# Optimization experiments

Measured on AMD Instinct MI355X. Metric: run time of the kernel, lower is better.

The kernel has to match this reference:

```python
import jax, jax.numpy as jnp
import numpy as np


def setup_inputs() -> dict:
    key = jax.random.key(0)
    k1, k2, k3, k4 = jax.random.split(key, 4)
    B, T, C, H = 4, 2048, 1024, 64
    x = jax.random.normal(k1, (B, T, C), dtype=jnp.float32)
    # Linear(embed_dim, head_size, bias=False) weights, stored as [C, H] for x @ W
    s = 1.0 / np.sqrt(C)
    Wq = jax.random.normal(k2, (C, H), dtype=jnp.float32) * s
    Wk = jax.random.normal(k3, (C, H), dtype=jnp.float32) * s
    Wv = jax.random.normal(k4, (C, H), dtype=jnp.float32) * s
    return {"x": x, "Wq": Wq, "Wk": Wk, "Wv": Wv}


def reference(x, Wq, Wk, Wv):
    B, T, C = x.shape
    q = x @ Wq  # [B, T, H]
    k = x @ Wk
    v = x @ Wv
    # NOTE: original scales by embed_dim**-0.5 (C), not head_size**-0.5
    scale = C ** (-0.5)
    wei = jnp.einsum("bqh,bkh->bqk", q, k) * scale  # [B, T, T]
    causal = jnp.tril(jnp.ones((T, T), dtype=bool))
    wei = jnp.where(causal, wei, -jnp.inf)
    wei = jax.nn.softmax(wei, axis=-1)
    # dropout_rate = 0 -> identity
    out = jnp.einsum("bqk,bkh->bqh", wei, v)  # [B, T, H]
    return out
```

## Files before the change

### kernel.cpp

```cpp
#include <hip/hip_runtime.h>
#include <cmath>

#define B_ 4
#define T_ 2048
#define C_ 1024
#define H_ 64
#define SCALE_ 0.03125f
#define NEG_ -3.0e38f

typedef __attribute__((ext_vector_type(4))) float f32x4;
typedef __attribute__((ext_vector_type(8))) short s16x8;
typedef __attribute__((ext_vector_type(4))) unsigned short u16x4;

__device__ inline unsigned short f2bf(float f) {
    union { float f; unsigned u; } v; v.f = f;
    unsigned r = v.u + 0x7FFFu + ((v.u >> 16) & 1u);
    return (unsigned short)(r >> 16);
}

#define LDK 72

__global__ __launch_bounds__(256) void proj_mfma(
    const float* __restrict__ x, const float* __restrict__ Wq,
    const float* __restrict__ Wk, const float* __restrict__ Wv,
    unsigned short* __restrict__ qb, unsigned short* __restrict__ kb,
    unsigned short* __restrict__ vt)
{
    __shared__ unsigned short As[64 * LDK];
    __shared__ unsigned short Bs[64 * LDK];

    const int t = threadIdx.x;
    const int lane = t & 63;
    const int w = t >> 6;
    const int blk = blockIdx.x;
    const int mat = blk % 3;
    const int row0 = (blk / 3) * 64;

    const float* W = (mat == 0) ? Wq : (mat == 1) ? Wk : Wv;

    const int wr = (w >> 1) * 32;
    const int wc = (w & 1) * 32;
    const int fr = lane & 15;
    const int ko = (lane >> 4) * 8;

    f32x4 acc[2][2];
    #pragma unroll
    for (int mi = 0; mi < 2; ++mi)
        #pragma unroll
        for (int ni = 0; ni < 2; ++ni)
            acc[mi][ni] = (f32x4){0.f, 0.f, 0.f, 0.f};

    const int bcol = t & 63;
    const int bkg  = (t >> 6) * 4;

    for (int kt = 0; kt < C_; kt += 64) {
        __syncthreads();
        #pragma unroll
        for (int i = 0; i < 4; ++i) {
            int idx = t + i * 256;
            int r = idx >> 4, kc = (idx & 15) * 4;
            f32x4 xv = *(const f32x4*)(x + (size_t)(row0 + r) * C_ + kt + kc);
            u16x4 bv;
            bv.x = f2bf(xv.x); bv.y = f2bf(xv.y); bv.z = f2bf(xv.z); bv.w = f2bf(xv.w);
            *(u16x4*)&As[r * LDK + kc] = bv;
        }
        #pragma unroll
        for (int i = 0; i < 4; ++i) {
            int kk0 = bkg + i * 16;
            u16x4 bv;
            bv.x = f2bf(W[(size_t)(kt + kk0 + 0) * H_ + bcol]);
            bv.y = f2bf(W[(size_t)(kt + kk0 + 1) * H_ + bcol]);
            bv.z = f2bf(W[(size_t)(kt + kk0 + 2) * H_ + bcol]);
            bv.w = f2bf(W[(size_t)(kt + kk0 + 3) * H_ + bcol]);
            *(u16x4*)&Bs[bcol * LDK + kk0] = bv;
        }
        __syncthreads();
        #pragma unroll
        for (int ks = 0; ks < 2; ++ks) {
            s16x8 a0 = *(const s16x8*)&As[(wr + fr) * LDK + ks * 32 + ko];
            s16x8 a1 = *(const s16x8*)&As[(wr + 16 + fr) * LDK + ks * 32 + ko];
            s16x8 b0 = *(const s16x8*)&Bs[(wc + fr) * LDK + ks * 32 + ko];
            s16x8 b1 = *(const s16x8*)&Bs[(wc + 16 + fr) * LDK + ks * 32 + ko];
            acc[0][0] = __builtin_amdgcn_mfma_f32_16x16x32_bf16(a0, b0, acc[0][0], 0, 0, 0);
            acc[0][1] = __builtin_amdgcn_mfma_f32_16x16x32_bf16(a0, b1, acc[0][1], 0, 0, 0);
            acc[1][0] = __builtin_amdgcn_mfma_f32_16x16x32_bf16(a1, b0, acc[1][0], 0, 0, 0);
            acc[1][1] = __builtin_amdgcn_mfma_f32_16x16x32_bf16(a1, b1, acc[1][1], 0, 0, 0);
        }
    }

    if (mat < 2) {
        unsigned short* outb = (mat == 0) ? qb : kb;
        #pragma unroll
        for (int mi = 0; mi < 2; ++mi)
            #pragma unroll
            for (int ni = 0; ni < 2; ++ni)
                #pragma unroll
                for (int j = 0; j < 4; ++j) {
                    int row = row0 + wr + mi * 16 + (lane >> 4) * 4 + j;
                    int col = wc + ni * 16 + fr;
                    outb[(size_t)row * H_ + col] = f2bf(acc[mi][ni][j]);
                }
    } else {
        __syncthreads();
        #pragma unroll
        for (int mi = 0; mi < 2; ++mi)
            #pragma unroll
            for (int ni = 0; ni < 2; ++ni)
                #pragma unroll
                for (int j = 0; j < 4; ++j) {
                    int r = wr + mi * 16 + (lane >> 4) * 4 + j;
                    int cc = wc + ni * 16 + fr;
                    As[cc * LDK + r] = f2bf(acc[mi][ni][j]);
                }
        __syncthreads();
        int h = t >> 2, c0 = (t & 3) * 16;
        int bb = row0 >> 11, trow = row0 & 2047;
        s16x8 v0 = *(const s16x8*)&As[h * LDK + c0];
        s16x8 v1 = *(const s16x8*)&As[h * LDK + c0 + 8];
        size_t dst = (size_t)bb * H_ * T_ + (size_t)h * T_ + trow + c0;
        *(s16x8*)&vt[dst] = v0;
        *(s16x8*)&vt[dst + 8] = v1;
    }
}

__global__ __launch_bounds__(512, 4) void attn_mfma(
    const unsigned short* __restrict__ qb, const unsigned short* __restrict__ kb,
    const unsigned short* __restrict__ vt, float* __restrict__ out)
{
    __shared__ alignas(16) unsigned short Ps[8][1024];
    __shared__ float Os[8][16][68];
    __shared__ float Mm[8][16];
    __shared__ float Ll[8][16];

    const int t = threadIdx.x, lane = t & 63, w = t >> 6;
    const int fr = lane & 15, hi4 = lane >> 4;
    const int blk = blockIdx.x;
    const int b = blk & 3;
    const int qt = 127 - (blk >> 2);
    const int qbase = qt * 16;

    const unsigned short* qp = qb + ((size_t)b * T_ + qbase) * H_;
    const unsigned short* kp = kb + (size_t)b * T_ * H_;
    const unsigned short* vp = vt + (size_t)b * H_ * T_;

    s16x8 qf0 = *(const s16x8*)&qp[fr * H_ + hi4 * 8];
    s16x8 qf1 = *(const s16x8*)&qp[fr * H_ + 32 + hi4 * 8];

    const int nt = (qbase + 79) >> 6;
    const int per = (nt + 7) >> 3;
    const int tb = w * per;
    int te = tb + per; if (te > nt) te = nt;

    float m = NEG_, l = 0.f;
    f32x4 o[4];
    #pragma unroll
    for (int hf = 0; hf < 4; ++hf) o[hf] = (f32x4){0.f, 0.f, 0.f, 0.f};

    unsigned short* P = &Ps[w][0];
    const int swz = (fr & 3) << 4;
    const int qrow = qbase + fr;

    for (int kt = tb; kt < te; ++kt) {
        const int kt0 = kt << 6;

        f32x4 s[4];
        #pragma unroll
        for (int n = 0; n < 4; ++n) {
            const unsigned short* kr = &kp[(size_t)(kt0 + n * 16 + fr) * H_ + hi4 * 8];
            s16x8 kf0 = *(const s16x8*)kr;
            s16x8 kf1 = *(const s16x8*)(kr + 32);
            f32x4 a = (f32x4){0.f, 0.f, 0.f, 0.f};
            a = __builtin_amdgcn_mfma_f32_16x16x32_bf16(kf0, qf0, a, 0, 0, 0);
            a = __builtin_amdgcn_mfma_f32_16x16x32_bf16(kf1, qf1, a, 0, 0, 0);
            s[n] = a;
        }

        if (kt0 + 63 > qbase) {
            #pragma unroll
            for (int n = 0; n < 4; ++n)
                #pragma unroll
                for (int j = 0; j < 4; ++j) {
                    int key = kt0 + n * 16 + hi4 * 4 + j;
                    float sv = s[n][j] * SCALE_;
                    s[n][j] = (key > qrow) ? NEG_ : sv;
                }
        } else {
            #pragma unroll
            for (int n = 0; n < 4; ++n)
                #pragma unroll
                for (int j = 0; j < 4; ++j) s[n][j] *= SCALE_;
        }

        float mx01 = fmaxf(fmaxf(s[0][0], s[0][1]), fmaxf(s[0][2], s[0][3]));
        float mx23 = fmaxf(fmaxf(s[1][0], s[1][1]), fmaxf(s[1][2], s[1][3]));
        float mx45 = fmaxf(fmaxf(s[2][0], s[2][1]), fmaxf(s[2][2], s[2][3]));
        float mx67 = fmaxf(fmaxf(s[3][0], s[3][1]), fmaxf(s[3][2], s[3][3]));
        float mx = fmaxf(fmaxf(mx01, mx23), fmaxf(mx45, mx67));
        mx = fmaxf(mx, __shfl_xor(mx, 16));
        mx = fmaxf(mx, __shfl_xor(mx, 32));

        float mn = fmaxf(m, mx);
        float corr = __expf(m - mn);
        m = mn;
        float sum = 0.f;
        #pragma unroll
        for (int n = 0; n < 4; ++n)
            #pragma unroll
            for (int j = 0; j < 4; ++j) {
                float p = __expf(s[n][j] - mn);
                s[n][j] = p; sum += p;
            }
        sum += __shfl_xor(sum, 16);
        sum += __shfl_xor(sum, 32);
        l = l * corr + sum;

        #pragma unroll
        for (int j = 0; j < 4; ++j) {
            float cj = __shfl(corr, (lane & 48) + hi4 * 4 + j);
            o[0][j] *= cj; o[1][j] *= cj; o[2][j] *= cj; o[3][j] *= cj;
        }

        #pragma unroll
        for (int n = 0; n < 4; ++n) {
            u16x4 pk;
            pk.x = f2bf(s[n][0]); pk.y = f2bf(s[n][1]);
            pk.z = f2bf(s[n][2]); pk.w = f2bf(s[n][3]);
            *(u16x4*)&P[fr * 64 + ((n * 16 + hi4 * 4) ^ swz)] = pk;
        }
        s16x8 pa0 = *(const s16x8*)&P[fr * 64 + ((hi4 * 8) ^ swz)];
        s16x8 pa1 = *(const s16x8*)&P[fr * 64 + ((32 + hi4 * 8) ^ swz)];

        #pragma unroll
        for (int hf = 0; hf < 4; ++hf) {
            const unsigned short* vr = &vp[(size_t)(hf * 16 + fr) * T_ + kt0 + hi4 * 8];
            s16x8 vf0 = *(const s16x8*)vr;
            s16x8 vf1 = *(const s16x8*)(vr + 32);
            o[hf] = __builtin_amdgcn_mfma_f32_16x16x32_bf16(pa0, vf0, o[hf], 0, 0, 0);
            o[hf] = __builtin_amdgcn_mfma_f32_16x16x32_bf16(pa1, vf1, o[hf], 0, 0, 0);
        }
    }

    if (hi4 == 0) { Mm[w][fr] = m; Ll[w][fr] = l; }
    #pragma unroll
    for (int hf = 0; hf < 4; ++hf)
        #pragma unroll
        for (int j = 0; j < 4; ++j)
            Os[w][hi4 * 4 + j][hf * 16 + fr] = o[hf][j];
    __syncthreads();

    if (t < 256) {
        int qq = t >> 4, h0 = (t & 15) * 4;
        float M = NEG_;
        #pragma unroll
        for (int s8 = 0; s8 < 8; ++s8) M = fmaxf(M, Mm[s8][qq]);
        float L = 0.f;
        f32x4 r = (f32x4){0.f, 0.f, 0.f, 0.f};
        #pragma unroll
        for (int s8 = 0; s8 < 8; ++s8) {
            float e = __expf(Mm[s8][qq] - M);
            L += Ll[s8][qq] * e;
            f32x4 osv = *(const f32x4*)&Os[s8][qq][h0];
            r.x = fmaf(osv.x, e, r.x);
            r.y = fmaf(osv.y, e, r.y);
            r.z = fmaf(osv.z, e, r.z);
            r.w = fmaf(osv.w, e, r.w);
        }
        float il = 1.0f / L;
        r.x *= il; r.y *= il; r.z *= il; r.w *= il;
        *(f32x4*)&out[((size_t)b * T_ + qbase + qq) * H_ + h0] = r;
    }
}

extern "C" void kernel_launch(void* const* d_in, const int* in_sizes, int n_in,
                              void* d_out, int out_size, void* d_ws, size_t ws_size,
                              hipStream_t stream) {
    const float* x  = (const float*)d_in[0];
    const float* Wq = (const float*)d_in[1];
    const float* Wk = (const float*)d_in[2];
    const float* Wv = (const float*)d_in[3];
    float* outp = (float*)d_out;

    unsigned short* base = (unsigned short*)d_ws;
    unsigned short* qbw = base;
    unsigned short* kbw = base + 524288;
    unsigned short* vtw = base + 1048576;

    proj_mfma<<<(B_ * T_ / 64) * 3, 256, 0, stream>>>(x, Wq, Wk, Wv, qbw, kbw, vtw);
    attn_mfma<<<B_ * (T_ / 16), 512, 0, stream>>>(qbw, kbw, vtw, outp);
}
```

Baseline: 49.57 us.

## Fold softmax scale into exp2, skip rescale under threshold, prefetch V fragments

The softmax scale and log2(e) are folded into one constant, so the kernel uses exp2f with an FMA and no longer scales the raw scores. The running max is updated and O/l rescaled only when some lane's new max exceeds the stored max by more than a threshold (lazy rescaling, FA4-style). V fragments are loaded before the softmax so their latency overlaps with the exp work, and bf16 conversion now uses the library intrinsic. The lazy rescale lets unnormalized values grow up to roughly 2^8 before a rescale is forced, which adds some numerical risk, and the early V loads raise register pressure.

```diff
diff --git a/kernel.cpp b/kernel.cpp
--- a/kernel.cpp
+++ b/kernel.cpp
@@ -1,4 +1,5 @@
 #include <hip/hip_runtime.h>
+#include <hip/hip_bf16.h>
 #include <cmath>
 
 #define B_ 4
@@ -6,6 +7,8 @@
 #define C_ 1024
 #define H_ 64
 #define SCALE_ 0.03125f
+#define K2_ 0.04508422003f
+#define THRRAW_ 177.0f
 #define NEG_ -3.0e38f
 
 typedef __attribute__((ext_vector_type(4))) float f32x4;
@@ -13,9 +16,9 @@
 typedef __attribute__((ext_vector_type(4))) unsigned short u16x4;
 
 __device__ inline unsigned short f2bf(float f) {
-    union { float f; unsigned u; } v; v.f = f;
-    unsigned r = v.u + 0x7FFFu + ((v.u >> 16) & 1u);
-    return (unsigned short)(r >> 16);
+    union { __hip_bfloat16 h; unsigned short u; } cv;
+    cv.h = __float2bfloat16(f);
+    return cv.u;
 }
 
 #define LDK 72
@@ -175,50 +178,53 @@
             s[n] = a;
         }
 
+        s16x8 vf[4][2];
+        #pragma unroll
+        for (int hf = 0; hf < 4; ++hf) {
+            const unsigned short* vr = &vp[(size_t)(hf * 16 + fr) * T_ + kt0 + hi4 * 8];
+            vf[hf][0] = *(const s16x8*)vr;
+            vf[hf][1] = *(const s16x8*)(vr + 32);
+        }
+
         if (kt0 + 63 > qbase) {
             #pragma unroll
             for (int n = 0; n < 4; ++n)
                 #pragma unroll
                 for (int j = 0; j < 4; ++j) {
                     int key = kt0 + n * 16 + hi4 * 4 + j;
-                    float sv = s[n][j] * SCALE_;
-                    s[n][j] = (key > qrow) ? NEG_ : sv;
+                    s[n][j] = (key > qrow) ? NEG_ : s[n][j];
                 }
-        } else {
-            #pragma unroll
-            for (int n = 0; n < 4; ++n)
-                #pragma unroll
-                for (int j = 0; j < 4; ++j) s[n][j] *= SCALE_;
-        }
-
-        float mx01 = fmaxf(fmaxf(s[0][0], s[0][1]), fmaxf(s[0][2], s[0][3]));
-        float mx23 = fmaxf(fmaxf(s[1][0], s[1][1]), fmaxf(s[1][2], s[1][3]));
-        float mx45 = fmaxf(fmaxf(s[2][0], s[2][1]), fmaxf(s[2][2], s[2][3]));
-        float mx67 = fmaxf(fmaxf(s[3][0], s[3][1]), fmaxf(s[3][2], s[3][3]));
-        float mx = fmaxf(fmaxf(mx01, mx23), fmaxf(mx45, mx67));
-        mx = fmaxf(mx, __shfl_xor(mx, 16));
-        mx = fmaxf(mx, __shfl_xor(mx, 32));
-
-        float mn = fmaxf(m, mx);
-        float corr = __expf(m - mn);
-        m = mn;
+        }
+
+        float mxl = fmaxf(fmaxf(fmaxf(fmaxf(s[0][0], s[0][1]), fmaxf(s[0][2], s[0][3])),
+                                fmaxf(fmaxf(s[1][0], s[1][1]), fmaxf(s[1][2], s[1][3]))),
+                          fmaxf(fmaxf(fmaxf(s[2][0], s[2][1]), fmaxf(s[2][2], s[2][3])),
+                                fmaxf(fmaxf(s[3][0], s[3][1]), fmaxf(s[3][2], s[3][3]))));
+        if (!__all(mxl - m <= THRRAW_)) {
+            float mx = fmaxf(mxl, __shfl_xor(mxl, 16));
+            mx = fmaxf(mx, __shfl_xor(mx, 32));
+            float mn = fmaxf(m, mx);
+            float corr = exp2f((m - mn) * K2_);
+            m = mn;
+            l *= corr;
+            #pragma unroll
+            for (int j = 0; j < 4; ++j) {
+                float cj = __shfl(corr, (lane & 48) + hi4 * 4 + j);
+                o[0][j] *= cj; o[1][j] *= cj; o[2][j] *= cj; o[3][j] *= cj;
+            }
+        }
+        const float nmk = -m * K2_;
         float sum = 0.f;
         #pragma unroll
         for (int n = 0; n < 4; ++n)
             #pragma unroll
             for (int j = 0; j < 4; ++j) {
-                float p = __expf(s[n][j] - mn);
+                float p = exp2f(fmaf(s[n][j], K2_, nmk));
                 s[n][j] = p; sum += p;
             }
         sum += __shfl_xor(sum, 16);
         sum += __shfl_xor(sum, 32);
-        l = l * corr + sum;
-
-        #pragma unroll
-        for (int j = 0; j < 4; ++j) {
-            float cj = __shfl(corr, (lane & 48) + hi4 * 4 + j);
-            o[0][j] *= cj; o[1][j] *= cj; o[2][j] *= cj; o[3][j] *= cj;
-        }
+        l += sum;
 
         #pragma unroll
         for (int n = 0; n < 4; ++n) {
@@ -232,11 +238,8 @@
 
         #pragma unroll
         for (int hf = 0; hf < 4; ++hf) {
-            const unsigned short* vr = &vp[(size_t)(hf * 16 + fr) * T_ + kt0 + hi4 * 8];
-            s16x8 vf0 = *(const s16x8*)vr;
-            s16x8 vf1 = *(const s16x8*)(vr + 32);
-            o[hf] = __builtin_amdgcn_mfma_f32_16x16x32_bf16(pa0, vf0, o[hf], 0, 0, 0);
-            o[hf] = __builtin_amdgcn_mfma_f32_16x16x32_bf16(pa1, vf1, o[hf], 0, 0, 0);
+            o[hf] = __builtin_amdgcn_mfma_f32_16x16x32_bf16(pa0, vf[hf][0], o[hf], 0, 0, 0);
+            o[hf] = __builtin_amdgcn_mfma_f32_16x16x32_bf16(pa1, vf[hf][1], o[hf], 0, 0, 0);
         }
     }
 
@@ -257,7 +260,7 @@
         f32x4 r = (f32x4){0.f, 0.f, 0.f, 0.f};
         #pragma unroll
         for (int s8 = 0; s8 < 8; ++s8) {
-            float e = __expf(Mm[s8][qq] - M);
+            float e = exp2f((Mm[s8][qq] - M) * K2_);
             L += Ll[s8][qq] * e;
             f32x4 osv = *(const f32x4*)&Os[s8][qq][h0];
             r.x = fmaf(osv.x, e, r.x);
```

Result: faster. 48.51 us (-2.1%).
